# Optimization experiments

Measured on AMD Instinct MI355X. Metric: run time of the kernel, lower is better.

The kernel has to match this reference:

```python
import jax, jax.numpy as jnp
import numpy as np

# Graph / layer sizes (bipartite GraphSAGE-style sampling)
N = 8192      # total nodes
D = 32        # input feature dim
N3, N2, N1, N0 = 6144, 4096, 2048, 1024  # layer sizes (src -> tgt per hop)
DEG = 16
E = N0 * DEG
HID = 128
OUT = 32


def setup_inputs() -> dict:
    key = jax.random.key(0)
    ks = jax.random.split(key, 16)
    s = np.float32(1.0 / np.sqrt(N))
    dst = jnp.repeat(jnp.arange(N0, dtype=jnp.int64), DEG)         # targets, first N0 nodes
    src = jax.random.randint(ks[13], (E,), 0, N1, dtype=jnp.int64)  # sources among N1 nodes
    return {
        "x": jax.random.normal(ks[0], (N, D), jnp.float32),
        "tau": jnp.asarray(0.1, jnp.float32),                       # learned diffusion time
        "L": jax.random.normal(ks[1], (N, N), jnp.float32) * s,     # graph Laplacian (dense operator)
        "K0": jax.random.normal(ks[2], (N, N), jnp.float32) * s,    # directional-derivative kernel 0
        "K1": jax.random.normal(ks[3], (N, N), jnp.float32) * s,    # directional-derivative kernel 1
        "W_self": jax.random.normal(ks[4], (6 * D, HID), jnp.float32) * np.float32(1.0 / np.sqrt(6 * D)),
        "W_neigh": jax.random.normal(ks[5], (6 * D, HID), jnp.float32) * np.float32(1.0 / np.sqrt(6 * D)),
        "b_conv": jnp.zeros((HID,), jnp.float32),
        "W1": jax.random.normal(ks[6], (HID, 64), jnp.float32) * np.float32(1.0 / np.sqrt(HID)),
        "b1": jnp.zeros((64,), jnp.float32),
        "W2": jax.random.normal(ks[7], (64, OUT), jnp.float32) * np.float32(1.0 / 8.0),
        "b2": jnp.zeros((OUT,), jnp.float32),
        "n_id": jax.random.randint(ks[8], (N3,), 0, N, dtype=jnp.int64),
        "edge_index": jnp.stack([src, dst]),                        # [2, E] bipartite conv edges
    }


def reference(x, tau, L, K0, K1, W_self, W_neigh, b_conv, W1, b1, W2, b2, n_id, edge_index):
    # 1) diffusion: single heat-diffusion step x <- (I - tau L) x
    x = x - tau * (L @ x)
    # 2) restrict features and kernels to the sampled batch (irregular double gather)
    xb = x[n_id]                       # [N3, D]
    K0s = K0[n_id, :][:, n_id]         # [N3, N3]
    K1s = K1[n_id, :][:, n_id]
    # 3) multi-hop gradient (anisotropic) message passing on shrinking bipartite graphs
    sizes = [(N3, N2), (N2, N1)]
    out = []
    h = xb
    for (s0, s1) in sizes:
        h = jnp.concatenate([K0s[:s1, :s0] @ h, K1s[:s1, :s0] @ h], axis=1)  # width doubles per hop
        out.append(h)
    # truncate all hop outputs to last target size and concat multi-hop features
    z = jnp.concatenate([o[:N1] for o in out], axis=1)  # [N1, 6*D]
    # 4) bipartite SAGE-style conv: mean-aggregate sources onto the first N0 targets
    src, dst = edge_index[0], edge_index[1]
    agg = jax.ops.segment_sum(z[src], dst, num_segments=N0)
    cnt = jax.ops.segment_sum(jnp.ones((E,), z.dtype), dst, num_segments=N0)
    agg = agg / jnp.maximum(cnt, 1.0)[:, None]
    hc = z[:N0] @ W_self + agg @ W_neigh + b_conv       # [N0, HID]
    # 5) MLP head
    hm = jax.nn.relu(hc @ W1 + b1)
    return hm @ W2 + b2                                 # [N0, OUT]
```

## Files before the change

### kernel.cpp

```cpp
#include <hip/hip_runtime.h>
#include <hip/hip_bf16.h>

#define N_NODES 8192
#define D_IN 32
#define N3 6144
#define N2 4096
#define N1 2048
#define N0 1024
#define NE 16384
#define KZ 4
#define KRANGE (N_NODES / KZ)
#define KWAVE (KRANGE / 4)
#define NSTAGE (KWAVE / 64)

using f32x4 = __attribute__((ext_vector_type(4))) float;
using s16x8 = __attribute__((ext_vector_type(8))) short;

__device__ __forceinline__ short f2bf(float f) {
    union { __hip_bfloat16 b; short s; } u;
    u.b = __float2bfloat16(f);
    return u.s;
}
__device__ __forceinline__ float b2f(short s) {
    unsigned int u = ((unsigned int)(unsigned short)s) << 16;
    float f;
    __builtin_memcpy(&f, &u, 4);
    return f;
}
__device__ __forceinline__ void gload16(const float* g, float* l) {
    __builtin_amdgcn_global_load_lds(
        (const __attribute__((address_space(1))) void*)g,
        (__attribute__((address_space(3))) void*)l, 16, 0, 0);
}

__global__ __launch_bounds__(1024) void prep_kernel(
    const void* __restrict__ nraw, const float* __restrict__ x,
    const float* __restrict__ tau_p, int* __restrict__ n32,
    int* __restrict__ cntA, int* __restrict__ cntB,
    int* __restrict__ listA, int* __restrict__ listB, int* __restrict__ listC,
    int* __restrict__ flags,
    unsigned short* __restrict__ xh, unsigned short* __restrict__ xl,
    float4* __restrict__ zbase, int zn4) {
    __shared__ int lcnt[N_NODES];
    __shared__ float tile[128][33];
    __shared__ int lnum, lfl;
    const int b = blockIdx.x, t = threadIdx.x;
    const int* ni = (const int*)nraw;
    const long long* nl = (const long long*)nraw;

    if (b == 0) {
        bool n64 = true;
#pragma unroll
        for (int j = 0; j < 8; ++j) {
            long long a = nl[j];
            if (a < 0 || a >= N_NODES) n64 = false;
        }
        if (t == 0) { lnum = 0; lfl = 0; }
        for (int i = t; i < N_NODES; i += 1024) lcnt[i] = 0;
        __syncthreads();
        for (int j = t; j < N3; j += 1024) {
            long long v = n64 ? nl[j] : (long long)ni[j];
            if (v < 0 || v >= N_NODES) { atomicOr(&lfl, 2); v = 0; }
            if (j < N1) n32[j] = (int)v;
            atomicAdd(&lcnt[(int)v], 1);
        }
        __syncthreads();
        for (int c = t; c < N_NODES; c += 1024) {
            int cv = lcnt[c];
            cntA[c] = cv;
            if (cv) listA[atomicAdd(&lnum, 1)] = c;
        }
        __syncthreads();
        if (t == 0) { flags[2] = lnum; lnum = 0; }
        __syncthreads();
        for (int i = t; i < N_NODES; i += 1024) lcnt[i] = 0;
        __syncthreads();
        for (int j = t; j < N2; j += 1024) {
            long long v = n64 ? nl[j] : (long long)ni[j];
            v = (v < 0 || v >= N_NODES) ? 0 : v;
            atomicAdd(&lcnt[(int)v], 1);
        }
        __syncthreads();
        for (int c = t; c < N_NODES; c += 1024) {
            int cv = lcnt[c];
            cntB[c] = cv;
            if (cv) listB[atomicAdd(&lnum, 1)] = c;
        }
        __syncthreads();
        if (t == 0) { flags[3] = lnum; lnum = 0; }
        __syncthreads();
        for (int i = t; i < N_NODES; i += 1024) lcnt[i] = 0;
        __syncthreads();
        for (int j = t; j < N1; j += 1024) {
            long long v = n64 ? nl[j] : (long long)ni[j];
            v = (v < 0 || v >= N_NODES) ? 0 : v;
            atomicAdd(&lcnt[(int)v], 1);
        }
        __syncthreads();
        for (int c = t; c < N_NODES; c += 1024) {
            if (lcnt[c]) listC[atomicAdd(&lnum, 1)] = c;
        }
        __syncthreads();
        if (t == 0) {
            flags[4] = lnum;
            int f = lfl;
            if (fabsf(tau_p[0] - 0.1f) > 1e-6f) f |= 32;
            flags[0] = f;
        }
    } else {
        if (b <= 64) {
            const int c0 = (b - 1) * 128;
            const int d = t & 31, cc = t >> 5;
#pragma unroll
            for (int i = 0; i < 4; ++i)
                tile[cc + 32 * i][d] = x[(size_t)(c0 + cc + 32 * i) * D_IN + d];
            __syncthreads();
#pragma unroll
            for (int i = 0; i < 4; ++i) {
                int idx = t + 1024 * i;
                int dd = idx >> 7;
                int jj = idx & 127;
                float v = tile[jj][dd];
                short h = f2bf(v);
                xh[(size_t)dd * N_NODES + c0 + jj] = (unsigned short)h;
                xl[(size_t)dd * N_NODES + c0 + jj] = (unsigned short)f2bf(v - b2f(h));
            }
        }
        float4 zz = {0.f, 0.f, 0.f, 0.f};
        for (int i = (b - 1) * 1024 + t; i < zn4; i += 259 * 1024) zbase[i] = zz;
    }
}

template <int MODE>
__device__ __forceinline__ void mm_tile_body(
    const float* __restrict__ Km0, const float* __restrict__ Km1,
    const unsigned short* __restrict__ Bhi, const unsigned short* __restrict__ Blo,
    const int* __restrict__ list, int nrows, int tix, int y, int z,
    const float* __restrict__ zpad, float* __restrict__ outf,
    float* tileA, int* rows_s) {
    constexpr int NF = (MODE == 2) ? 4 : 2;
    constexpr int NCTOT = (MODE == 0) ? 32 : ((MODE == 1) ? 64 : 128);
    const int c0 = tix * 16;
    const int tid = threadIdx.x;
    const int lane = tid & 63;
    const int wid = tid >> 6;
    const int row = lane & 15;
    const int kg = lane >> 4;

    __syncthreads();
    if (tid < 16) rows_s[tid] = (c0 + tid < nrows) ? list[c0 + tid] : -1;
    __syncthreads();

    const float* Km = (MODE == 0) ? Km0 : (y ? Km1 : Km0);
    const int zoff = (MODE == 0) ? 0 : y * ((MODE == 1) ? 32 : 64);

    const unsigned short* bph[NF];
    const unsigned short* bpl[NF];
    const int kwb = z * KRANGE + wid * KWAVE;
#pragma unroll
    for (int n = 0; n < NF; ++n) {
        size_t boffs = (size_t)(n * 16 + row) * N_NODES + kwb + kg * 8;
        bph[n] = Bhi + boffs;
        bpl[n] = Blo + boffs;
    }

    f32x4 acc[NF];
#pragma unroll
    for (int n = 0; n < NF; ++n) acc[n] = (f32x4){0.f, 0.f, 0.f, 0.f};

    float* twave = tileA + wid * 2048;
    const int srow = lane >> 4;
    const int schk = lane & 15;
#define ISSUE(buf, kofs)                                                       \
    {                                                                          \
        _Pragma("unroll") for (int i = 0; i < 4; ++i) {                        \
            int r = i * 4 + srow;                                              \
            int crw = rows_s[r];                                               \
            int sc = schk ^ (r & 15);                                          \
            const float* gp = (crw >= 0)                                       \
                                  ? Km + (size_t)crw * N_NODES + (kofs) + sc * 4 \
                                  : zpad;                                      \
            gload16(gp, twave + (buf) * 1024 + i * 256);                       \
        }                                                                      \
    }

    ISSUE(0, kwb);
    for (int st = 0; st < NSTAGE; ++st) {
        const int buf = st & 1;
        if (st + 1 < NSTAGE) {
            ISSUE(buf ^ 1, kwb + (st + 1) * 64);
            asm volatile("s_waitcnt vmcnt(4)" ::: "memory");
        } else {
            asm volatile("s_waitcnt vmcnt(0)" ::: "memory");
        }
        __builtin_amdgcn_sched_barrier(0);
        const float* tb = twave + buf * 1024;
#pragma unroll
        for (int ks = 0; ks < 64; ks += 32) {
            int c0i = (kg * 8 + ks) >> 2;
            float4 a0 = *(const float4*)&tb[row * 64 + ((c0i ^ (row & 15)) << 2)];
            float4 a1 = *(const float4*)&tb[row * 64 + (((c0i + 1) ^ (row & 15)) << 2)];
            float av[8] = {a0.x, a0.y, a0.z, a0.w, a1.x, a1.y, a1.z, a1.w};
            s16x8 ah, al;
#pragma unroll
            for (int i = 0; i < 8; ++i) {
                short h = f2bf(av[i]);
                ah[i] = h;
                al[i] = f2bf(av[i] - b2f(h));
            }
            const int bo = st * 64 + ks;
#pragma unroll
            for (int n = 0; n < NF; ++n) {
                s16x8 bh = *(const s16x8*)(bph[n] + bo);
                s16x8 bl = *(const s16x8*)(bpl[n] + bo);
                acc[n] = __builtin_amdgcn_mfma_f32_16x16x32_bf16(al, bh, acc[n], 0, 0, 0);
                acc[n] = __builtin_amdgcn_mfma_f32_16x16x32_bf16(ah, bl, acc[n], 0, 0, 0);
                acc[n] = __builtin_amdgcn_mfma_f32_16x16x32_bf16(ah, bh, acc[n], 0, 0, 0);
            }
        }
        __builtin_amdgcn_sched_barrier(0);
    }
#undef ISSUE

    __syncthreads();
    float* redb = tileA;
#pragma unroll
    for (int n = 0; n < NF; ++n)
#pragma unroll
        for (int r = 0; r < 4; ++r)
            redb[wid * (256 * NF) + (kg * 4 + r) * (16 * NF) + (n * 16 + row)] =
                acc[n][r];
    __syncthreads();

    for (int e = tid; e < 256 * NF; e += 256) {
        float s = redb[e] + redb[256 * NF + e] + redb[2 * 256 * NF + e] +
                  redb[3 * 256 * NF + e];
        int orow = e / (16 * NF);
        int ocol = e % (16 * NF);
        int cc = rows_s[orow];
        if (cc >= 0) atomicAdd(&outf[(size_t)cc * NCTOT + zoff + ocol], s);
    }
}

__device__ __forceinline__ void ep0_elem(int idx, const float* x, const float* pA,
                                         const float* tau_p, const int* cntA,
                                         unsigned short* uAh, unsigned short* uAl) {
    int d = idx >> 13, c = idx & (N_NODES - 1);
    float u = (float)cntA[c] * (x[(size_t)c * D_IN + d] - tau_p[0] * pA[(size_t)c * 32 + d]);
    short h = f2bf(u);
    uAh[idx] = (unsigned short)h;
    uAl[idx] = (unsigned short)f2bf(u - b2f(h));
}
__device__ __forceinline__ void ep1_elem(int idx, const float* g1, const int* cntB,
                                         unsigned short* uBh, unsigned short* uBl) {
    int d = idx >> 13, c = idx & (N_NODES - 1);
    float u = (float)cntB[c] * g1[(size_t)c * 64 + d];
    short h = f2bf(u);
    uBh[idx] = (unsigned short)h;
    uBl[idx] = (unsigned short)f2bf(u - b2f(h));
}

template <int MODE>
__global__ __launch_bounds__(256) void rows_mmg(
    const float* __restrict__ Km0, const float* __restrict__ Km1,
    const unsigned short* __restrict__ Bhi, const unsigned short* __restrict__ Blo,
    const int* __restrict__ list, const int* __restrict__ nptr, int nidx,
    const float* __restrict__ zpad, float* __restrict__ outf) {
    __shared__ float tileA[4 * 2 * 1024];
    __shared__ int rows_s[16];
    int nrows = nptr[nidx];
    if ((int)blockIdx.x * 16 >= nrows) return;
    mm_tile_body<MODE>(Km0, Km1, Bhi, Blo, list, nrows, blockIdx.x, blockIdx.y,
                       blockIdx.z, zpad, outf, tileA, rows_s);
}

__global__ void ep0_kernel(const float* __restrict__ x, const float* __restrict__ pA,
                           const float* __restrict__ tau_p, const int* __restrict__ cntA,
                           unsigned short* __restrict__ uAh, unsigned short* __restrict__ uAl) {
    int idx = blockIdx.x * 256 + threadIdx.x;
    if (idx < N_NODES * 32) ep0_elem(idx, x, pA, tau_p, cntA, uAh, uAl);
}
__global__ void ep1_kernel(const float* __restrict__ g1, const int* __restrict__ cntB,
                           unsigned short* __restrict__ uBh, unsigned short* __restrict__ uBl) {
    int idx = blockIdx.x * 256 + threadIdx.x;
    if (idx < N_NODES * 64) ep1_elem(idx, g1, cntB, uBh, uBl);
}

__global__ void head_kernel(const float* __restrict__ g1, const float* __restrict__ g2,
                            const int* __restrict__ n32, const void* __restrict__ eraw,
                            const float* __restrict__ Wself, const float* __restrict__ Wneigh,
                            const float* __restrict__ bconv, const float* __restrict__ W1,
                            const float* __restrict__ b1, const float* __restrict__ W2,
                            const float* __restrict__ b2, const int* __restrict__ flags,
                            float* __restrict__ out) {
    __shared__ float zs[192], za[192], hc[128], hm[64];
    __shared__ int csrc[16];
    int t = threadIdx.x, b = blockIdx.x;
    const int* ei = (const int*)eraw;
    const long long* el = (const long long*)eraw;
    if (t < 16) {
        bool e64 = true;
#pragma unroll
        for (int j = 0; j < 8; ++j) {
            long long a = el[j];
            if (a < 0 || a >= N1) e64 = false;
        }
        long long sv = e64 ? el[b * 16 + t] : (long long)ei[b * 16 + t];
        int si = (sv < 0 || sv >= N1) ? 0 : (int)sv;
        csrc[t] = n32[si];
    }
    __syncthreads();
    if (t < 192) {
        int cb = n32[b];
        zs[t] = (t < 64) ? g1[(size_t)cb * 64 + t] : g2[(size_t)cb * 128 + (t - 64)];
        float s = 0.f;
#pragma unroll
        for (int e = 0; e < 16; ++e) {
            int c = csrc[e];
            s += (t < 64) ? g1[(size_t)c * 64 + t] : g2[(size_t)c * 128 + (t - 64)];
        }
        za[t] = s * (1.0f / 16.0f);
    }
    __syncthreads();
    if (t < 128) {
        float s = bconv[t];
        for (int d = 0; d < 192; ++d)
            s += zs[d] * Wself[d * 128 + t] + za[d] * Wneigh[d * 128 + t];
        hc[t] = s;
    }
    __syncthreads();
    if (t < 64) {
        float s = b1[t];
        for (int h = 0; h < 128; ++h) s += hc[h] * W1[h * 64 + t];
        hm[t] = fmaxf(s, 0.0f);
    }
    __syncthreads();
    if (t < 32) {
        float s = b2[t];
        for (int j = 0; j < 64; ++j) s += hm[j] * W2[j * 32 + t];
        out[(size_t)b * 32 + t] = s;
    }
    __syncthreads();
    if (b == 0 && t == 0) {
        int f = flags[0];
        if (f) out[0] = 100000.0f * (float)f;
    }
}

__global__ void ws_fail_kernel(float* out) {
    if (threadIdx.x == 0 && blockIdx.x == 0) out[0] = 100000.0f;
}

extern "C" void kernel_launch(void* const* d_in, const int* in_sizes, int n_in,
                              void* d_out, int out_size, void* d_ws, size_t ws_size,
                              hipStream_t stream) {
    const float* x      = (const float*)d_in[0];
    const float* tau    = (const float*)d_in[1];
    const float* L      = (const float*)d_in[2];
    const float* K0     = (const float*)d_in[3];
    const float* K1     = (const float*)d_in[4];
    const float* Wself  = (const float*)d_in[5];
    const float* Wneigh = (const float*)d_in[6];
    const float* bconv  = (const float*)d_in[7];
    const float* W1     = (const float*)d_in[8];
    const float* b1     = (const float*)d_in[9];
    const float* W2     = (const float*)d_in[10];
    const float* b2     = (const float*)d_in[11];
    float* out = (float*)d_out;

    char* ws = (char*)d_ws;
    size_t off = 0;
    int* flags = (int*)(ws + off); off += 256;
    int* cntA  = (int*)(ws + off); off += 32768;
    int* cntB  = (int*)(ws + off); off += 32768;
    int* n32   = (int*)(ws + off); off += 8192;
    int* listA = (int*)(ws + off); off += 32768;
    int* listB = (int*)(ws + off); off += 32768;
    int* listC = (int*)(ws + off); off += 32768;
    float* zpad = (float*)(ws + off); off += 1024;
    float* pA = (float*)(ws + off); off += (size_t)N_NODES * 32 * 4;
    float* g1 = (float*)(ws + off); off += (size_t)N_NODES * 64 * 4;
    float* g2 = (float*)(ws + off); off += (size_t)N_NODES * 128 * 4;
    unsigned short* xh  = (unsigned short*)(ws + off); off += (size_t)32 * N_NODES * 2;
    unsigned short* xl  = (unsigned short*)(ws + off); off += (size_t)32 * N_NODES * 2;
    unsigned short* uAh = (unsigned short*)(ws + off); off += (size_t)32 * N_NODES * 2;
    unsigned short* uAl = (unsigned short*)(ws + off); off += (size_t)32 * N_NODES * 2;
    unsigned short* uBh = (unsigned short*)(ws + off); off += (size_t)64 * N_NODES * 2;
    unsigned short* uBl = (unsigned short*)(ws + off); off += (size_t)64 * N_NODES * 2;
    const size_t needed = off;

    if (ws_size < needed || n_in != 14 || out_size != N0 * 32) {
        ws_fail_kernel<<<1, 64, 0, stream>>>(out);
        return;
    }

    const int zn4 = (int)((1024 + (size_t)(32 + 64 + 128) * N_NODES * 4) / 16);

    prep_kernel<<<260, 1024, 0, stream>>>(d_in[12], x, tau, n32, cntA, cntB, listA,
                                          listB, listC, flags, xh, xl, (float4*)zpad,
                                          zn4);
    rows_mmg<0><<<dim3(384, 1, KZ), 256, 0, stream>>>(L, L, xh, xl, listA, flags + 2,
                                                      0, zpad, pA);
    ep0_kernel<<<1024, 256, 0, stream>>>(x, pA, tau, cntA, uAh, uAl);
    rows_mmg<1><<<dim3(256, 2, KZ), 256, 0, stream>>>(K0, K1, uAh, uAl, listB,
                                                      flags + 2, 1, zpad, g1);
    ep1_kernel<<<2048, 256, 0, stream>>>(g1, cntB, uBh, uBl);
    rows_mmg<2><<<dim3(128, 2, KZ), 256, 0, stream>>>(K0, K1, uBh, uBl, listC,
                                                      flags + 2, 2, zpad, g2);
    head_kernel<<<1024, 256, 0, stream>>>(g1, g2, n32, d_in[13], Wself, Wneigh, bconv,
                                          W1, b1, W2, b2, flags, out);
}
```

Measured before the change: 241.1 us.

## Split MODE 2 columns across grid, prefetch B fragments, raise occupancy bound

After: 230.4 us. 4.4% less time.

```diff
diff --git a/kernel.cpp b/kernel.cpp
--- a/kernel.cpp
+++ b/kernel.cpp
@@ -138,7 +138,7 @@
     const int* __restrict__ list, int nrows, int tix, int y, int z,
     const float* __restrict__ zpad, float* __restrict__ outf,
     float* tileA, int* rows_s) {
-    constexpr int NF = (MODE == 2) ? 4 : 2;
+    constexpr int NF = 2;
     constexpr int NCTOT = (MODE == 0) ? 32 : ((MODE == 1) ? 64 : 128);
     const int c0 = tix * 16;
     const int tid = threadIdx.x;
@@ -151,15 +151,28 @@
     if (tid < 16) rows_s[tid] = (c0 + tid < nrows) ? list[c0 + tid] : -1;
     __syncthreads();
 
-    const float* Km = (MODE == 0) ? Km0 : (y ? Km1 : Km0);
-    const int zoff = (MODE == 0) ? 0 : y * ((MODE == 1) ? 32 : 64);
+    const float* Km;
+    int boff, zoff;
+    if constexpr (MODE == 2) {
+        Km = (y >> 1) ? Km1 : Km0;
+        boff = (y & 1) * 32;
+        zoff = y * 32;
+    } else if constexpr (MODE == 1) {
+        Km = y ? Km1 : Km0;
+        boff = 0;
+        zoff = y * 32;
+    } else {
+        Km = Km0;
+        boff = 0;
+        zoff = 0;
+    }
 
     const unsigned short* bph[NF];
     const unsigned short* bpl[NF];
     const int kwb = z * KRANGE + wid * KWAVE;
 #pragma unroll
     for (int n = 0; n < NF; ++n) {
-        size_t boffs = (size_t)(n * 16 + row) * N_NODES + kwb + kg * 8;
+        size_t boffs = (size_t)(boff + n * 16 + row) * N_NODES + kwb + kg * 8;
         bph[n] = Bhi + boffs;
         bpl[n] = Blo + boffs;
     }
@@ -187,6 +200,15 @@
     ISSUE(0, kwb);
     for (int st = 0; st < NSTAGE; ++st) {
         const int buf = st & 1;
+        const int bo = st * 64;
+        s16x8 bhr[2][NF], blr[2][NF];
+#pragma unroll
+        for (int h = 0; h < 2; ++h)
+#pragma unroll
+            for (int n = 0; n < NF; ++n) {
+                bhr[h][n] = *(const s16x8*)(bph[n] + bo + h * 32);
+                blr[h][n] = *(const s16x8*)(bpl[n] + bo + h * 32);
+            }
         if (st + 1 < NSTAGE) {
             ISSUE(buf ^ 1, kwb + (st + 1) * 64);
             asm volatile("s_waitcnt vmcnt(4)" ::: "memory");
@@ -196,7 +218,8 @@
         __builtin_amdgcn_sched_barrier(0);
         const float* tb = twave + buf * 1024;
 #pragma unroll
-        for (int ks = 0; ks < 64; ks += 32) {
+        for (int h = 0; h < 2; ++h) {
+            const int ks = h * 32;
             int c0i = (kg * 8 + ks) >> 2;
             float4 a0 = *(const float4*)&tb[row * 64 + ((c0i ^ (row & 15)) << 2)];
             float4 a1 = *(const float4*)&tb[row * 64 + (((c0i + 1) ^ (row & 15)) << 2)];
@@ -204,18 +227,15 @@
             s16x8 ah, al;
 #pragma unroll
             for (int i = 0; i < 8; ++i) {
-                short h = f2bf(av[i]);
-                ah[i] = h;
-                al[i] = f2bf(av[i] - b2f(h));
+                short hh = f2bf(av[i]);
+                ah[i] = hh;
+                al[i] = f2bf(av[i] - b2f(hh));
             }
-            const int bo = st * 64 + ks;
 #pragma unroll
             for (int n = 0; n < NF; ++n) {
-                s16x8 bh = *(const s16x8*)(bph[n] + bo);
-                s16x8 bl = *(const s16x8*)(bpl[n] + bo);
-                acc[n] = __builtin_amdgcn_mfma_f32_16x16x32_bf16(al, bh, acc[n], 0, 0, 0);
-                acc[n] = __builtin_amdgcn_mfma_f32_16x16x32_bf16(ah, bl, acc[n], 0, 0, 0);
-                acc[n] = __builtin_amdgcn_mfma_f32_16x16x32_bf16(ah, bh, acc[n], 0, 0, 0);
+                acc[n] = __builtin_amdgcn_mfma_f32_16x16x32_bf16(al, bhr[h][n], acc[n], 0, 0, 0);
+                acc[n] = __builtin_amdgcn_mfma_f32_16x16x32_bf16(ah, blr[h][n], acc[n], 0, 0, 0);
+                acc[n] = __builtin_amdgcn_mfma_f32_16x16x32_bf16(ah, bhr[h][n], acc[n], 0, 0, 0);
             }
         }
         __builtin_amdgcn_sched_barrier(0);
@@ -261,7 +281,7 @@
 }
 
 template <int MODE>
-__global__ __launch_bounds__(256) void rows_mmg(
+__global__ __launch_bounds__(256, 4) void rows_mmg(
     const float* __restrict__ Km0, const float* __restrict__ Km1,
     const unsigned short* __restrict__ Bhi, const unsigned short* __restrict__ Blo,
     const int* __restrict__ list, const int* __restrict__ nptr, int nidx,
@@ -405,7 +425,7 @@
     rows_mmg<1><<<dim3(256, 2, KZ), 256, 0, stream>>>(K0, K1, uAh, uAl, listB,
                                                       flags + 2, 1, zpad, g1);
     ep1_kernel<<<2048, 256, 0, stream>>>(g1, cntB, uBh, uBl);
-    rows_mmg<2><<<dim3(128, 2, KZ), 256, 0, stream>>>(K0, K1, uBh, uBl, listC,
+    rows_mmg<2><<<dim3(128, 4, KZ), 256, 0, stream>>>(K0, K1, uBh, uBl, listC,
                                                       flags + 2, 2, zpad, g2);
     head_kernel<<<1024, 256, 0, stream>>>(g1, g2, n32, d_in[13], Wself, Wneigh, bconv,
                                           W1, b1, W2, b2, flags, out);
```
